# Kernel optimization log

Measured on AMD Instinct MI355X. Metric: run time of the kernel, lower is better.

The kernel has to match this reference:

```python
import jax, jax.numpy as jnp
import numpy as np

N = 100000          # nodes
E = 800000          # edges per relation
R = 6               # relations
B = 1000            # graphs
IN_DIM = 14
POS_COL = 5
PE = 8              # pos_emb_dim
H = 128             # hidden_dim
OUT = 128           # out_dim
NPOS = 24
D1 = IN_DIM - 1 + PE  # 21, GAT layer-1 input dim


def setup_inputs() -> dict:
    key = jax.random.key(0)
    ks = jax.random.split(key, 20)
    x_all = jax.random.normal(ks[0], (N, IN_DIM), dtype=jnp.float32)
    pos = jax.random.randint(ks[1], (N,), 0, NPOS)
    x_all = x_all.at[:, POS_COL].set(pos.astype(jnp.float32))
    edges = jax.random.randint(ks[2], (R, 2, E), 0, N, dtype=jnp.int32)
    batch = jnp.sort(jax.random.randint(ks[3], (N,), 0, B, dtype=jnp.int32))
    pos_table = jax.random.normal(ks[4], (NPOS, PE), dtype=jnp.float32) * 0.02
    W1 = jax.random.normal(ks[5], (R, D1, H), dtype=jnp.float32) * 0.1
    as1 = jax.random.normal(ks[6], (R, H), dtype=jnp.float32) * 0.1
    ad1 = jax.random.normal(ks[7], (R, H), dtype=jnp.float32) * 0.1
    b1 = jnp.zeros((R, H), dtype=jnp.float32)
    W2 = jax.random.normal(ks[8], (R, H, H), dtype=jnp.float32) * 0.05
    as2 = jax.random.normal(ks[9], (R, H), dtype=jnp.float32) * 0.1
    ad2 = jax.random.normal(ks[10], (R, H), dtype=jnp.float32) * 0.1
    b2 = jnp.zeros((R, H), dtype=jnp.float32)
    n1w = jnp.ones((H,), dtype=jnp.float32)
    n1b = jnp.zeros((H,), dtype=jnp.float32)
    n2w = jnp.ones((H,), dtype=jnp.float32)
    n2b = jnp.zeros((H,), dtype=jnp.float32)
    query = jax.random.normal(ks[11], (H,), dtype=jnp.float32) * 0.02
    projW = jax.random.normal(ks[12], (H, OUT), dtype=jnp.float32) * 0.05
    projb = jnp.zeros((OUT,), dtype=jnp.float32)
    return dict(x_all=x_all, edges=edges, batch=batch, pos_table=pos_table,
                W1=W1, as1=as1, ad1=ad1, b1=b1, W2=W2, as2=as2, ad2=ad2, b2=b2,
                n1w=n1w, n1b=n1b, n2w=n2w, n2b=n2b, query=query, projW=projW, projb=projb)


def _seg_softmax(logits, seg, num):
    m = jax.lax.stop_gradient(jax.ops.segment_max(logits, seg, num_segments=num))
    e = jnp.exp(logits - m[seg])
    s = jax.ops.segment_sum(e, seg, num_segments=num)
    return e / s[seg]


def _gat_layer(x, W, a_s, a_d, b, edges):
    # sum over R relation-specific GATConv(heads=1, concat=False) outputs
    n = x.shape[0]
    out = jnp.zeros((n, W.shape[-1]), dtype=x.dtype)
    for r in range(R):
        xp = x @ W[r]                       # [N, H] projected features
        src, dst = edges[r, 0], edges[r, 1]
        z = (xp @ a_s[r])[src] + (xp @ a_d[r])[dst]
        z = jnp.where(z > 0, z, 0.2 * z)    # LeakyReLU(0.2)
        alpha = _seg_softmax(z, dst, n)     # per-destination softmax
        agg = jax.ops.segment_sum(alpha[:, None] * xp[src], dst, num_segments=n)
        out = out + agg + b[r]
    return out


def _ln(x, w, b):
    mu = x.mean(-1, keepdims=True)
    v = ((x - mu) ** 2).mean(-1, keepdims=True)
    return (x - mu) / jnp.sqrt(v + 1e-5) * w + b


def reference(x_all, edges, batch, pos_table, W1, as1, ad1, b1,
              W2, as2, ad2, b2, n1w, n1b, n2w, n2b, query, projW, projb):
    cont = jnp.concatenate([x_all[:, :POS_COL], x_all[:, POS_COL + 1:]], axis=1)
    pidx = jnp.clip(x_all[:, POS_COL].astype(jnp.int32), 0, NPOS - 1)
    x = jnp.concatenate([cont, pos_table[pidx]], axis=1)  # [N, D1]
    x = _gat_layer(x, W1, as1, ad1, b1, edges)
    x = _ln(jax.nn.gelu(x, approximate=False), n1w, n1b)
    x = _gat_layer(x, W2, as2, ad2, b2, edges)
    x = _ln(jax.nn.gelu(x, approximate=False), n2w, n2b)
    # AttentionPooling: gather-score-softmax-scatter over batch segments
    scores = x @ query
    w = _seg_softmax(scores, batch, B)
    pool = jax.ops.segment_sum(w[:, None] * x, batch, num_segments=B)  # [B, H]
    return pool @ projW + projb
```

## Files before the change

### kernel.cpp

```cpp
#include <hip/hip_runtime.h>
#include <math.h>

#define NN   100000
#define EE   800000
#define RR   6
#define BB   1000
#define HH   128
#define MM   (RR*NN)
#define NBPR ((NN + 255) >> 8)
#define NBK  (RR * NBPR)
#define CH   4096
#define CAP  4096

static inline int ceil_div(int a, int b){ return (a+b-1)/b; }

typedef __attribute__((ext_vector_type(8))) short bf16x8;
typedef __attribute__((ext_vector_type(4))) short bf16x4;
typedef __attribute__((ext_vector_type(4))) float f32x4;

__device__ __forceinline__ unsigned fenc(float f){
  unsigned u = __float_as_uint(f);
  return (u & 0x80000000u) ? ~u : (u | 0x80000000u);
}
__device__ __forceinline__ float fdec(unsigned u){
// ... 32 lines not shown
  __syncthreads();
  for (int i = e0 + t; i < e1; i += 256) {
    int dst = dptr[i];
    int b = dst >> 8;
    int slot = base[b] + atomicAdd(&hist[b], 1);
    ebkt[slot] = ((unsigned)sptr[i] << 8) | (unsigned)(dst & 255);
  }
}

__global__ void k_bscan(const int* __restrict__ bcur, int* __restrict__ boff,
                        int* __restrict__ off)
{
  __shared__ int sh[256];
  int t = threadIdx.x;
  int carry = 0;
  for (int c = 0; c < NBK; c += 256) {
    int idx = c + t;
    int v = (idx < NBK) ? bcur[idx] : 0;
    sh[t] = v;
    __syncthreads();
    for (int o = 1; o < 256; o <<= 1) {
      int add = (t >= o) ? sh[t-o] : 0;
      __syncthreads();
      sh[t] += add;
      __syncthreads();
    }
    int incl = sh[t];
    int tot  = sh[255];
    if (idx < NBK) boff[idx] = carry + incl - v;
    __syncthreads();
    carry += tot;
  }
  if (t == 0) { boff[NBK] = carry; off[MM] = carry; }
}

__global__ void k_bbuild(const unsigned* __restrict__ ebkt, const int* __restrict__ bcur,
                         const int* __restrict__ boff,
                         int* __restrict__ off, int* __restrict__ elist)
{
  __shared__ int cnt[256];
  __shared__ int sc[256];
  __shared__ int cur[256];
  int t = threadIdx.x;
  int bb = blockIdx.x;
  int e0r = bb*CAP, e1r = e0r + bcur[bb];
  int w0 = boff[bb];
  cnt[t] = 0;
  __syncthreads();
  for (int i = e0r + t; i < e1r; i += 256)
    atomicAdd(&cnt[ebkt[i] & 255u], 1);
  __syncthreads();
  sc[t] = cnt[t];
  __syncthreads();
  for (int o = 1; o < 256; o <<= 1) {
    int add = (t >= o) ? sc[t-o] : 0;
    __syncthreads();
    sc[t] += add;
    __syncthreads();
  }
  int excl = sc[t] - cnt[t];
  int r = bb / NBPR, b = bb - r*NBPR;
  int dst = b*256 + t;
  if (dst < NN) off[r*NN + dst] = w0 + excl;
  cur[t] = w0 + excl;
  __syncthreads();
  for (int i = e0r + t; i < e1r; i += 256) {
    unsigned w = ebkt[i];
    int slot = atomicAdd(&cur[w & 255u], 1);
    elist[slot] = (int)(w >> 8);
  }
}

__global__ void k_featprep(const float* __restrict__ x_all, const float* __restrict__ pos_table,
                           short* __restrict__ x0h, short* __restrict__ x0l)
{
  int gid = blockIdx.x*256 + threadIdx.x;
  if (gid >= NN*32) return;
  int nidx = gid >> 5, c = gid & 31;
  float v = 0.f;
  if (c < 13) {
    int scl = (c < 5) ? c : c + 1;
    v = x_all[nidx*14 + scl];
  } else if (c < 21) {
    int pi = (int)x_all[nidx*14 + 5];
    pi = pi < 0 ? 0 : (pi > 23 ? 23 : pi);
    v = pos_table[pi*8 + (c - 13)];
  }
  unsigned short h = f2bf(v);
  unsigned short l = f2bf(v - bf2f(h));
  x0h[gid] = (short)h;
  x0l[gid] = (short)l;
}

template<int KP>
__global__ void k_wprep(const float* __restrict__ W, int K,
                        short* __restrict__ Wh, short* __restrict__ Wl)
{
  int gid = blockIdx.x*256 + threadIdx.x;
  if (gid >= RR*128*KP) return;
  int r = gid / (128*KP);
  int rem = gid - r*(128*KP);
  int nn = rem / KP, k = rem - nn*KP;
  float v = (k < K) ? W[((size_t)r*K + k)*128 + nn] : 0.f;
  unsigned short h = f2bf(v);
  unsigned short l = f2bf(v - bf2f(h));
  Wh[gid] = (short)h;
  Wl[gid] = (short)l;
}

template<int KP>
__global__ void k_wa(const float* __restrict__ W, const float* __restrict__ as,
                     const float* __restrict__ ad, int K, float* __restrict__ wa)
{
  int idx = blockIdx.x*256 + threadIdx.x;
  if (idx >= 12*KP) return;
  int rr = idx / KP, k = idx - rr*KP;
  int r = (rr < 6) ? rr : rr - 6;
  const float* a = ((rr < 6) ? as : ad) + (size_t)r*HH;
  float s = 0.f;
  if (k < K) {
    const float* wrow = W + ((size_t)r*K + k)*128;
    #pragma unroll 8
    for (int h = 0; h < 128; ++h) s = fmaf(wrow[h], a[h], s);
  }
  wa[idx] = s;
}

__global__ void k_zsd32(const short* __restrict__ xh, const short* __restrict__ xl,
                        const float* __restrict__ wa, float* __restrict__ zsd, int n)
{
  __shared__ float w[12*32];
  int tid = threadIdx.x;
  for (int i = tid; i < 12*32; i += 256) w[i] = wa[i];
  __syncthreads();
  int g = blockIdx.x*256 + tid;
  if (g >= n) return;
  float v[32];
  #pragma unroll
  for (int c = 0; c < 4; ++c) {
    uint4 vh = *(const uint4*)(xh + (size_t)g*32 + c*8);
    uint4 vl = *(const uint4*)(xl + (size_t)g*32 + c*8);
    const unsigned short* hp = (const unsigned short*)&vh;
    const unsigned short* lp = (const unsigned short*)&vl;
    #pragma unroll
    for (int j = 0; j < 8; ++j) v[c*8+j] = bf2f(hp[j]) + bf2f(lp[j]);
  }
  #pragma unroll
  for (int rr = 0; rr < 12; ++rr) {
    float d = 0.f;
    #pragma unroll
    for (int k = 0; k < 32; ++k) d = fmaf(v[k], w[rr*32+k], d);
    zsd[(size_t)rr*n + g] = d;
  }
}

__global__ void k_agg1(const unsigned short* __restrict__ x0h, const float* __restrict__ zsd,
                       const int* __restrict__ elist, const int* __restrict__ off,
                       unsigned short* __restrict__ aggH, unsigned short* __restrict__ aggL,
                       int n)
{
  int gid = blockIdx.x*256 + threadIdx.x;
  int g = gid >> 4;
  int l = threadIdx.x & 15;
  if (g >= n) return;
  int sub = l >> 2, ch = l & 3;

  for (int rel = 0; rel < RR; ++rel) {
    const float* zsr = zsd + (size_t)rel*n;
    const float* zdr = zsd + (size_t)(6+rel)*n;
    int o0 = off[(size_t)rel*NN + g];
    int deg = off[(size_t)rel*NN + g + 1] - o0;
    float acc[8] = {0,0,0,0,0,0,0,0};
    float inv = 0.f;
    if (deg > 0) {
      float zdd = zdr[g];
      float m = -3.4e38f, es = 0.f;
      for (int i = l; i < deg; i += 16) {
        float z = zsr[elist[o0+i]] + zdd;
        z = (z > 0.f) ? z : 0.2f*z;
        float mn = fmaxf(m, z);
        es = es*__expf(m - mn) + __expf(z - mn);
        m = mn;
      }
      #pragma unroll
      for (int o = 1; o <= 8; o <<= 1) {
        float mo = __shfl_xor(m, o), eo = __shfl_xor(es, o);
        float mn = fmaxf(m, mo);
        es = es*__expf(m - mn) + eo*__expf(mo - mn);
        m = mn;
      }
      inv = 1.f / es;
      for (int base = 0; base < deg; base += 8) {
        int i0 = base + sub, i1 = base + 4 + sub;
        float e0 = 0.f, e1 = 0.f; int s0 = 0, s1 = 0;
        if (i0 < deg) {
          s0 = elist[o0+i0];
          float z = zsr[s0] + zdd;
          z = (z > 0.f) ? z : 0.2f*z;
          e0 = __expf(z - m);
        }
        if (i1 < deg) {
          s1 = elist[o0+i1];
          float z = zsr[s1] + zdd;
          z = (z > 0.f) ? z : 0.2f*z;
          e1 = __expf(z - m);
        }
        uint4 v0 = *(const uint4*)(x0h + (size_t)s0*32 + ch*8);
        uint4 v1 = *(const uint4*)(x0h + (size_t)s1*32 + ch*8);
        acc[0] = fmaf(e0, __uint_as_float(v0.x << 16),         acc[0]);
        acc[1] = fmaf(e0, __uint_as_float(v0.x & 0xffff0000u), acc[1]);
        acc[2] = fmaf(e0, __uint_as_float(v0.y << 16),         acc[2]);
        acc[3] = fmaf(e0, __uint_as_float(v0.y & 0xffff0000u), acc[3]);
        acc[4] = fmaf(e0, __uint_as_float(v0.z << 16),         acc[4]);
        acc[5] = fmaf(e0, __uint_as_float(v0.z & 0xffff0000u), acc[5]);
        acc[6] = fmaf(e0, __uint_as_float(v0.w << 16),         acc[6]);
        acc[7] = fmaf(e0, __uint_as_float(v0.w & 0xffff0000u), acc[7]);
        acc[0] = fmaf(e1, __uint_as_float(v1.x << 16),         acc[0]);
        acc[1] = fmaf(e1, __uint_as_float(v1.x & 0xffff0000u), acc[1]);
        acc[2] = fmaf(e1, __uint_as_float(v1.y << 16),         acc[2]);
        acc[3] = fmaf(e1, __uint_as_float(v1.y & 0xffff0000u), acc[3]);
        acc[4] = fmaf(e1, __uint_as_float(v1.z << 16),         acc[4]);
        acc[5] = fmaf(e1, __uint_as_float(v1.z & 0xffff0000u), acc[5]);
        acc[6] = fmaf(e1, __uint_as_float(v1.w << 16),         acc[6]);
        acc[7] = fmaf(e1, __uint_as_float(v1.w & 0xffff0000u), acc[7]);
      }
      #pragma unroll
      for (int j = 0; j < 8; ++j) {
        acc[j] += __shfl_xor(acc[j], 4);
        acc[j] += __shfl_xor(acc[j], 8);
      }
    }
    if (sub == 0) {
      uint4 ph, pl;
      unsigned* php = (unsigned*)&ph; unsigned* plp = (unsigned*)&pl;
      #pragma unroll
      for (int j2 = 0; j2 < 4; ++j2) {
        float a0 = acc[2*j2]   * inv;
        float a1 = acc[2*j2+1] * inv;
        unsigned short h0 = f2bf(a0), h1 = f2bf(a1);
        php[j2] = ((unsigned)h1 << 16) | h0;
        plp[j2] = ((unsigned)f2bf(a1 - bf2f(h1)) << 16) | f2bf(a0 - bf2f(h0));
      }
      size_t o = ((size_t)rel*n + g)*32 + ch*8;
      *(uint4*)(aggH + o) = ph;
      *(uint4*)(aggL + o) = pl;
    }
  }
}

__device__ __forceinline__ bf16x8 ldfragG(const short* __restrict__ p, int row, int kb, int KP_)
{
  bf16x4 a = *(const bf16x4*)(p + (size_t)row*KP_ + kb);
  bf16x4 b = *(const bf16x4*)(p + (size_t)row*KP_ + kb + 16);
  return __builtin_shufflevector(a, b, 0,1,2,3,4,5,6,7);
}

__global__ __launch_bounds__(256, 4)
void k_gemm1(const short* __restrict__ aggH, const short* __restrict__ aggL,
             const short* __restrict__ Wh, const short* __restrict__ Wl,
             const float* __restrict__ bsv,
             const float* __restrict__ nw, const float* __restrict__ nb,
             unsigned short* __restrict__ Yh, int n)
{
  __shared__ __align__(16) float Cs[32*136];
  int tid = threadIdx.x;
  int r0 = blockIdx.x * 32;
  int wid = tid >> 6, lane = tid & 63;
  int lr = lane & 15, lg = lane >> 4;
  int rt = wid >> 1;
  int c0 = (wid & 1) * 4;
  int arow = r0 + rt*16 + lr;
  int kb = 4*lg;
  f32x4 acct[4] = {{0,0,0,0},{0,0,0,0},{0,0,0,0},{0,0,0,0}};

  for (int rel = 0; rel < RR; ++rel) {
    const short* Ahr = aggH + (size_t)rel*n*32;
    const short* Alr = aggL + (size_t)rel*n*32;
    const short* Whr = Wh + (size_t)rel*128*32;
    const short* Wlr = Wl + (size_t)rel*128*32;
    bf16x8 ah = ldfragG(Ahr, arow, kb, 32);
    bf16x8 al = ldfragG(Alr, arow, kb, 32);
    #pragma unroll
    for (int t = 0; t < 4; ++t) {
      int wrow = (c0 + t)*16 + lr;
      bf16x8 whf = ldfragG(Whr, wrow, kb, 32);
      bf16x8 wlf = ldfragG(Wlr, wrow, kb, 32);
      acct[t] = __builtin_amdgcn_mfma_f32_16x16x32_bf16(ah, whf, acct[t], 0, 0, 0);
      acct[t] = __builtin_amdgcn_mfma_f32_16x16x32_bf16(al, whf, acct[t], 0, 0, 0);
      acct[t] = __builtin_amdgcn_mfma_f32_16x16x32_bf16(ah, wlf, acct[t], 0, 0, 0);
    }
  }

  #pragma unroll
  for (int t = 0; t < 4; ++t)
    #pragma unroll
    for (int v = 0; v < 4; ++v) {
      int row = rt*16 + lg*4 + v;
      int col = (c0 + t)*16 + lr;
      float x = acct[t][v] + bsv[col];
      Cs[row*136 + col] = 0.5f*x*(1.f + erff(x*0.70710678118654752f));
    }
  __syncthreads();
  {
    int r = tid >> 3, sg = tid & 7;
    float vals[16];
    float s = 0.f;
    #pragma unroll
    for (int i = 0; i < 16; ++i) { vals[i] = Cs[r*136 + sg*16 + i]; s += vals[i]; }
    s += __shfl_xor(s, 1); s += __shfl_xor(s, 2); s += __shfl_xor(s, 4);
    float mu = s * (1.f/128.f);
    float var = 0.f;
    #pragma unroll
    for (int i = 0; i < 16; ++i) { vals[i] -= mu; var += vals[i]*vals[i]; }
    var += __shfl_xor(var, 1); var += __shfl_xor(var, 2); var += __shfl_xor(var, 4);
    float inv = 1.f / sqrtf(var*(1.f/128.f) + 1e-5f);
    int g = r0 + r;
    uint4 ph0, ph1;
    unsigned* php0 = (unsigned*)&ph0; unsigned* php1 = (unsigned*)&ph1;
    #pragma unroll
    for (int j2 = 0; j2 < 8; ++j2) {
      int c = sg*16 + 2*j2;
      float y0 = vals[2*j2]  *inv*nw[c]   + nb[c];
      float y1 = vals[2*j2+1]*inv*nw[c+1] + nb[c+1];
      unsigned hw = ((unsigned)f2bf(y1) << 16) | f2bf(y0);
      if (j2 < 4) php0[j2] = hw; else php1[j2-4] = hw;
    }
    *(uint4*)(Yh + (size_t)g*128 + sg*16)     = ph0;
    *(uint4*)(Yh + (size_t)g*128 + sg*16 + 8) = ph1;
  }
}

__device__ __forceinline__ bf16x8 ldfrag_(const short* p, int row, int kb, int KP_, int smask)
{
  int xr = row & smask;
  int s0 = (((kb)      >> 3) ^ xr) * 8 + (kb & 7);
  int s1 = (((kb + 16) >> 3) ^ xr) * 8 + (kb & 7);
  bf16x4 a = *(const bf16x4*)(p + (size_t)row*KP_ + s0);
  bf16x4 b = *(const bf16x4*)(p + (size_t)row*KP_ + s1);
  return __builtin_shufflevector(a, b, 0,1,2,3,4,5,6,7);
}

template<int KP>
__global__ __launch_bounds__(256, 2)
void k_gemm_mfma(const short* __restrict__ Ah,
                 const short* __restrict__ WhAll, const short* __restrict__ WlAll,
                 const float* __restrict__ a_sAll, const float* __restrict__ a_dAll,
                 unsigned short* __restrict__ xpbAll, float* __restrict__ zsAll,
                 float* __restrict__ zdAll, int rbase, int n)
{
  constexpr int SLOTS = KP/8;
  constexpr int SMASK = (SLOTS >= 8) ? 7 : (SLOTS-1);
  __shared__ short lds[288*KP];
  constexpr int AH0 = 0, WH0 = 32*KP, WL0 = 160*KP;
  int tid = threadIdx.x;
  int r0 = blockIdx.x * 32;
  int ry = blockIdx.y;
  const short* Wh = WhAll + (size_t)(rbase+ry)*128*KP;
  const short* Wl = WlAll + (size_t)(rbase+ry)*128*KP;
  const float* a_s = a_sAll + (size_t)(rbase+ry)*HH;
  const float* a_d = a_dAll + (size_t)(rbase+ry)*HH;
  unsigned short* xpb = xpbAll + (size_t)ry*n*128;
  float* zs = zsAll + (size_t)ry*n;
  float* zd = zdAll + (size_t)ry*n;

  for (int ch = tid; ch < 32*SLOTS; ch += 256) {
    int row = ch / SLOTS, slot = ch - row*SLOTS;
    int gr = r0 + row;
    int dsl = (slot ^ (row & SMASK)) * 8;
    bf16x8 vh;
    if (gr < n) {
      vh = *(const bf16x8*)(Ah + (size_t)gr*KP + slot*8);
    } else {
      #pragma unroll
      for (int q = 0; q < 8; ++q) vh[q] = 0;
    }
    *(bf16x8*)(lds + AH0 + row*KP + dsl) = vh;
  }
  for (int ch = tid; ch < 128*SLOTS; ch += 256) {
    int row = ch / SLOTS, slot = ch - row*SLOTS;
    int dsl = (slot ^ (row & SMASK)) * 8;
    *(bf16x8*)(lds + WH0 + row*KP + dsl) = *(const bf16x8*)(Wh + (size_t)row*KP + slot*8);
    *(bf16x8*)(lds + WL0 + row*KP + dsl) = *(const bf16x8*)(Wl + (size_t)row*KP + slot*8);
  }
  __syncthreads();

  int wid = tid >> 6, lane = tid & 63;
  int lr = lane & 15, lg = lane >> 4;
  int rt = wid >> 1;
  int c0 = (wid & 1) * 4;
  f32x4 acc[4] = {{0,0,0,0},{0,0,0,0},{0,0,0,0},{0,0,0,0}};
  int arow = rt*16 + lr;

  #pragma unroll
  for (int kc = 0; kc < KP/32; ++kc) {
    int kb = kc*32 + 4*lg;
    bf16x8 ah = ldfrag_(lds + AH0, arow, kb, KP, SMASK);
    #pragma unroll
    for (int t = 0; t < 4; ++t) {
      int wrow = (c0 + t)*16 + lr;
      bf16x8 wh = ldfrag_(lds + WH0, wrow, kb, KP, SMASK);
      bf16x8 wl = ldfrag_(lds + WL0, wrow, kb, KP, SMASK);
      acc[t] = __builtin_amdgcn_mfma_f32_16x16x32_bf16(ah, wh, acc[t], 0, 0, 0);
      acc[t] = __builtin_amdgcn_mfma_f32_16x16x32_bf16(ah, wl, acc[t], 0, 0, 0);
    }
  }
  __syncthreads();

  float* Cs = (float*)lds;
  #pragma unroll
  for (int t = 0; t < 4; ++t)
    #pragma unroll
    for (int v = 0; v < 4; ++v) {
      int row = rt*16 + lg*4 + v;
      int col = (c0 + t)*16 + lr;
      Cs[row*136 + col] = acc[t][v];
    }
  __syncthreads();

  {
    int r = tid >> 3, sg = tid & 7;
    float ps = 0.f, pd = 0.f;
    #pragma unroll
    for (int i = 0; i < 16; ++i) {
      int c = sg*16 + i;
      float x = Cs[r*136 + c];
      ps = fmaf(x, a_s[c], ps);
      pd = fmaf(x, a_d[c], pd);
    }
    ps += __shfl_xor(ps, 1); pd += __shfl_xor(pd, 1);
    ps += __shfl_xor(ps, 2); pd += __shfl_xor(pd, 2);
    ps += __shfl_xor(ps, 4); pd += __shfl_xor(pd, 4);
    int gr = r0 + r;
    if (sg == 0 && gr < n) { zs[gr] = ps; zd[gr] = pd; }
  }
  for (int i = tid; i < 32*16; i += 256) {
    int row = i >> 4, q = i & 15;
    int gr = r0 + row;
    if (gr < n) {
      const float* cp = Cs + row*136 + q*8;
      uint4 o;
      o.x = ((unsigned)f2bf(cp[1]) << 16) | f2bf(cp[0]);
      o.y = ((unsigned)f2bf(cp[3]) << 16) | f2bf(cp[2]);
      o.z = ((unsigned)f2bf(cp[5]) << 16) | f2bf(cp[4]);
      o.w = ((unsigned)f2bf(cp[7]) << 16) | f2bf(cp[6]);
      *(uint4*)(xpb + (size_t)gr*128 + q*8) = o;
    }
  }
}

#define ACC8(W_, U_) \
  tmp[0] = fmaf(W_, __uint_as_float((U_).x << 16),         tmp[0]); \
  tmp[1] = fmaf(W_, __uint_as_float((U_).x & 0xffff0000u), tmp[1]); \
  tmp[2] = fmaf(W_, __uint_as_float((U_).y << 16),         tmp[2]); \
  tmp[3] = fmaf(W_, __uint_as_float((U_).y & 0xffff0000u), tmp[3]); \
  tmp[4] = fmaf(W_, __uint_as_float((U_).z << 16),         tmp[4]); \
  tmp[5] = fmaf(W_, __uint_as_float((U_).z & 0xffff0000u), tmp[5]); \
  tmp[6] = fmaf(W_, __uint_as_float((U_).w << 16),         tmp[6]); \
  tmp[7] = fmaf(W_, __uint_as_float((U_).w & 0xffff0000u), tmp[7]);

template<int NREL, int FIN>
__global__ void k_agg3(const unsigned short* __restrict__ xpb,
                       const float* __restrict__ zs,
                       const float* __restrict__ zd,
                       const int* __restrict__ elist,
                       const int* __restrict__ off,
                       float* __restrict__ hacc,
                       const float* __restrict__ bsum,
                       const float* __restrict__ nw, const float* __restrict__ nb,
                       float* __restrict__ Yf,
                       const float* __restrict__ q,
                       const int* __restrict__ batch,
                       float* __restrict__ scores, unsigned* __restrict__ bmax,
                       int n)
{
  int gid = blockIdx.x*256 + threadIdx.x;
  int g = gid >> 4;
  int l = threadIdx.x & 15;
  int gbase = threadIdx.x & 48;
  if (g >= n) return;

  float acc[8] = {0,0,0,0,0,0,0,0};

  for (int r = 0; r < NREL; ++r) {
    int o0 = off[(size_t)r*NN + g], o1 = off[(size_t)r*NN + g + 1];
    int deg = o1 - o0;
    if (deg <= 0) continue;
    const float* zsr = zs + (size_t)r*n;
    float zdd = zd[(size_t)r*n + g];

    float m = -3.4e38f;
    for (int i = l; i < deg; i += 16) {
      float z = zsr[elist[o0+i]] + zdd;
      z = (z > 0.f) ? z : 0.2f*z;
      m = fmaxf(m, z);
    }
    m = fmaxf(m, __shfl_xor(m, 1));
    m = fmaxf(m, __shfl_xor(m, 2));
    m = fmaxf(m, __shfl_xor(m, 4));
    m = fmaxf(m, __shfl_xor(m, 8));

    float tmp[8] = {0,0,0,0,0,0,0,0};
    float esum = 0.f;
    const unsigned short* xr = xpb + (size_t)r*n*128;
    for (int base = 0; base < deg; base += 16) {
      int i = base + l;
      float ew = 0.f; int s = 0;
      if (i < deg) {
        s = elist[o0+i];
        float z = zsr[s] + zdd;
        z = (z > 0.f) ? z : 0.2f*z;
        ew = __expf(z - m);
      }
      esum += ew;
      int cnt = min(16, deg - base);
      for (int t = 0; t < cnt; t += 4) {
        float w0 = __shfl(ew, gbase + t);
        float w1 = __shfl(ew, gbase + t + 1);
        float w2 = __shfl(ew, gbase + t + 2);
        float w3 = __shfl(ew, gbase + t + 3);
        int a0 = __shfl(s, gbase + t);
        int a1 = __shfl(s, gbase + t + 1);
        int a2 = __shfl(s, gbase + t + 2);
        int a3 = __shfl(s, gbase + t + 3);
        uint4 u0 = *(const uint4*)(xr + (size_t)a0*128 + l*8);
        uint4 u1 = *(const uint4*)(xr + (size_t)a1*128 + l*8);
        uint4 u2 = *(const uint4*)(xr + (size_t)a2*128 + l*8);
        uint4 u3 = *(const uint4*)(xr + (size_t)a3*128 + l*8);
        ACC8(w0, u0);
        ACC8(w1, u1);
        ACC8(w2, u2);
        ACC8(w3, u3);
      }
    }
    esum += __shfl_xor(esum, 1);
    esum += __shfl_xor(esum, 2);
    esum += __shfl_xor(esum, 4);
    esum += __shfl_xor(esum, 8);
    float inv = 1.f / esum;
    #pragma unroll
    for (int j = 0; j < 8; ++j) acc[j] = fmaf(tmp[j], inv, acc[j]);
  }

  if (FIN == 0) {
    float* hp = hacc + (size_t)g*128 + l*8;
    float4 o0; o0.x = acc[0]; o0.y = acc[1]; o0.z = acc[2]; o0.w = acc[3];
    float4 o1; o1.x = acc[4]; o1.y = acc[5]; o1.z = acc[6]; o1.w = acc[7];
    *(float4*)hp = o0;
    *(float4*)(hp + 4) = o1;
  } else {
    if (FIN == 2) {
      const float* hp = hacc + (size_t)g*128 + l*8;
      float4 p0 = *(const float4*)hp;
      float4 p1 = *(const float4*)(hp + 4);
      acc[0] += p0.x; acc[1] += p0.y; acc[2] += p0.z; acc[3] += p0.w;
      acc[4] += p1.x; acc[5] += p1.y; acc[6] += p1.z; acc[7] += p1.w;
    }
    float4 b0 = *(const float4*)(bsum + l*8);
    float4 b1 = *(const float4*)(bsum + l*8 + 4);
    acc[0] += b0.x; acc[1] += b0.y; acc[2] += b0.z; acc[3] += b0.w;
    acc[4] += b1.x; acc[5] += b1.y; acc[6] += b1.z; acc[7] += b1.w;
    float s = 0.f;
    #pragma unroll
    for (int j = 0; j < 8; ++j) {
      acc[j] = 0.5f*acc[j]*(1.f + erff(acc[j]*0.70710678118654752f));
      s += acc[j];
    }
    s += __shfl_xor(s, 1); s += __shfl_xor(s, 2);
    s += __shfl_xor(s, 4); s += __shfl_xor(s, 8);
    float mu = s * (1.f/128.f);
    float v = 0.f;
    #pragma unroll
    for (int j = 0; j < 8; ++j) { acc[j] -= mu; v += acc[j]*acc[j]; }
    v += __shfl_xor(v, 1); v += __shfl_xor(v, 2);
    v += __shfl_xor(v, 4); v += __shfl_xor(v, 8);
    v *= (1.f/128.f);
    float inv = 1.f / sqrtf(v + 1e-5f);
    float4 w0 = *(const float4*)(nw + l*8);
    float4 w1 = *(const float4*)(nw + l*8 + 4);
    float4 nb0 = *(const float4*)(nb + l*8);
    float4 nb1 = *(const float4*)(nb + l*8 + 4);
    float y[8];
    y[0] = acc[0]*inv*w0.x + nb0.x; y[1] = acc[1]*inv*w0.y + nb0.y;
    y[2] = acc[2]*inv*w0.z + nb0.z; y[3] = acc[3]*inv*w0.w + nb0.w;
    y[4] = acc[4]*inv*w1.x + nb1.x; y[5] = acc[5]*inv*w1.y + nb1.y;
    y[6] = acc[6]*inv*w1.z + nb1.z; y[7] = acc[7]*inv*w1.w + nb1.w;
    float* yp = Yf + (size_t)g*128 + l*8;
    float4 o0; o0.x = y[0]; o0.y = y[1]; o0.z = y[2]; o0.w = y[3];
    float4 o1; o1.x = y[4]; o1.y = y[5]; o1.z = y[6]; o1.w = y[7];
    *(float4*)yp = o0;
    *(float4*)(yp + 4) = o1;
    float4 q0 = *(const float4*)(q + l*8);
    float4 q1 = *(const float4*)(q + l*8 + 4);
    float sc = y[0]*q0.x + y[1]*q0.y + y[2]*q0.z + y[3]*q0.w
             + y[4]*q1.x + y[5]*q1.y + y[6]*q1.z + y[7]*q1.w;
    sc += __shfl_xor(sc, 1); sc += __shfl_xor(sc, 2);
    sc += __shfl_xor(sc, 4); sc += __shfl_xor(sc, 8);
    if (l == 0) {
      scores[g] = sc;
      atomicMax(&bmax[batch[g]], fenc(sc));
    }
  }
}

__global__ void k_bsum(const float* __restrict__ b, float* __restrict__ bs)
{
  int t = threadIdx.x;
  float s = 0.f;
  #pragma unroll
  for (int r = 0; r < RR; ++r) s += b[r*HH + t];
  bs[t] = s;
}

__global__ void k_segbounds(const int* __restrict__ batch, int* __restrict__ segst,
                            int n, int numB)
{
  int b = blockIdx.x*256 + threadIdx.x;
  if (b > numB) return;
  int lo = 0, hi = n;
  while (lo < hi) { int mid = (lo+hi) >> 1; if (batch[mid] < b) lo = mid+1; else hi = mid; }
  segst[b] = lo;
}

__global__ void k_pool(const float* __restrict__ X, const float* __restrict__ scores,
                       const int* __restrict__ segst, const unsigned* __restrict__ bmax,
                       float* __restrict__ pool, int numB)
{
  int b = blockIdx.x;
  int t = threadIdx.x;
  int s0 = segst[b], s1 = segst[b+1];
  float m = fdec(bmax[b]);
  float acc0 = 0.f, acc1 = 0.f, esum = 0.f;
  int i = s0;
  for (; i + 1 < s1; i += 2) {
    float e0 = __expf(scores[i] - m);
    float e1 = __expf(scores[i+1] - m);
    esum += e0 + e1;
    acc0 = fmaf(e0, X[(size_t)i*128 + t], acc0);
    acc1 = fmaf(e1, X[(size_t)(i+1)*128 + t], acc1);
  }
  if (i < s1) {
    float e0 = __expf(scores[i] - m);
    esum += e0;
    acc0 = fmaf(e0, X[(size_t)i*128 + t], acc0);
  }
  float inv = (s1 > s0) ? 1.f/esum : 0.f;
  pool[(size_t)b*128 + t] = (acc0 + acc1) * inv;
}

__global__ void k_outgemm(const float* __restrict__ pool, const float* __restrict__ projW,
                          const float* __restrict__ projb, float* __restrict__ out, int numB)
{
  int b = blockIdx.x;
  int j = threadIdx.x;
  __shared__ float p[128];
  p[j] = pool[(size_t)b*128 + j];
  __syncthreads();
  float acc = projb[j];
  #pragma unroll 16
  for (int k = 0; k < 128; ++k) acc = fmaf(p[k], projW[(size_t)k*128 + j], acc);
  out[(size_t)b*128 + j] = acc;
}

extern "C" void kernel_launch(void* const* d_in, const int* in_sizes, int n_in,
                              void* d_out, int out_size, void* d_ws, size_t ws_size,
                              hipStream_t stream)
{
  const float* x_all = (const float*)d_in[0];
  const int*   edges = (const int*)d_in[1];
  const int*   batch = (const int*)d_in[2];
  const float* pos_table = (const float*)d_in[3];
  const float* W1  = (const float*)d_in[4];
  const float* as1 = (const float*)d_in[5];
  const float* ad1 = (const float*)d_in[6];
  const float* b1  = (const float*)d_in[7];
  const float* W2  = (const float*)d_in[8];
  const float* as2 = (const float*)d_in[9];
  const float* ad2 = (const float*)d_in[10];
  const float* b2  = (const float*)d_in[11];
  const float* n1w = (const float*)d_in[12];
  const float* n1b = (const float*)d_in[13];
  const float* n2w = (const float*)d_in[14];
  const float* n2b = (const float*)d_in[15];
  const float* query = (const float*)d_in[16];
  const float* projW = (const float*)d_in[17];
  const float* projb = (const float*)d_in[18];
  float* out = (float*)d_out;
  (void)in_sizes; (void)n_in; (void)out_size;

  auto asz = [](size_t b){ return (b + 255) & ~(size_t)255; };
  size_t baseNeed =
      asz((size_t)(MM+1)*4) + asz((size_t)RR*EE*4) + asz((size_t)(NBK+1)*4) +
      asz((size_t)NBK*4) + 2*asz((size_t)RR*128*128*2) + asz((size_t)12*128*4) +
      asz((size_t)12*NN*4) + asz(128*4) + asz((size_t)(BB+1)*4) + asz((size_t)BB*4) +
      asz((size_t)BB*HH*4) + asz((size_t)NN*4) +
      asz((size_t)NN*128*4)  + asz((size_t)NN*128*4) ;
  size_t need6 = baseNeed + asz((size_t)6*NN*128*2);
  const bool use6 = ws_size >= need6;

  char* p = (char*)d_ws;
  auto alloc = [&](size_t b){ void* r = (void*)p; p += (b + 255) & ~(size_t)255; return r; };
  int*   off   = (int*)alloc((size_t)(MM+1)*sizeof(int));
  int*   elist = (int*)alloc((size_t)RR*EE*sizeof(int));
  int*   boff  = (int*)alloc((size_t)(NBK+1)*sizeof(int));
  int*   bcur  = (int*)alloc((size_t)NBK*sizeof(int));
  short* wtH   = (short*)alloc((size_t)RR*128*128*sizeof(short));
  short* wtL   = (short*)alloc((size_t)RR*128*128*sizeof(short));
  float* wa    = (float*)alloc((size_t)12*128*sizeof(float));
  float* zsd   = (float*)alloc((size_t)12*NN*sizeof(float));
  float* bsv   = (float*)alloc(128*sizeof(float));
  int*   segst = (int*)alloc((size_t)(BB+1)*sizeof(int));
  unsigned* bmax = (unsigned*)alloc((size_t)BB*sizeof(unsigned));
  float* pool  = (float*)alloc((size_t)BB*HH*sizeof(float));
  float* scrs  = (float*)alloc((size_t)NN*sizeof(float));
  size_t xpbRel = use6 ? 6 : 3;
  unsigned short* xpb = (unsigned short*)alloc((size_t)xpbRel*NN*128*sizeof(short));
  float* R1    = (float*)alloc((size_t)NN*128*sizeof(float));
  float* R2    = (float*)alloc((size_t)NN*128*sizeof(float));

  unsigned* ebkt = (unsigned*)R1;
  short* x0h = (short*)R1;
  short* x0l = x0h + (size_t)NN*32;
  float* hacc = R1;
  unsigned short* h1h = (unsigned short*)R2;
  float* h2 = (float*)R2;
  unsigned short* aggH = (unsigned short*)xpb;
  unsigned short* aggL = aggH + (size_t)RR*NN*32;
  float* zs = zsd;
  float* zd = zsd + (use6 ? (size_t)6*NN : (size_t)3*NN);

  const int nch = (EE + CH - 1) / CH;
  hipMemsetAsync(bcur, 0, (size_t)NBK*sizeof(int), stream);
  k_binscatter<<<RR*nch,256,0,stream>>>(edges, bcur, ebkt);
  k_bscan<<<1,256,0,stream>>>(bcur, boff, off);
  k_bbuild<<<NBK,256,0,stream>>>(ebkt, bcur, boff, off, elist);

  k_featprep<<<ceil_div(NN*32,256),256,0,stream>>>(x_all, pos_table, x0h, x0l);
  k_segbounds<<<ceil_div(BB+1,256),256,0,stream>>>(batch, segst, NN, BB);
  hipMemsetAsync(bmax, 0, (size_t)BB*sizeof(unsigned), stream);

  k_wa<32><<<ceil_div(12*32,256),256,0,stream>>>(W1, as1, ad1, 21, wa);
  k_zsd32<<<ceil_div(NN,256),256,0,stream>>>(x0h, x0l, wa, zsd, NN);
  k_wprep<32><<<ceil_div(RR*128*32,256),256,0,stream>>>(W1, 21, wtH, wtL);
  k_bsum<<<1,128,0,stream>>>(b1, bsv);
  k_agg1<<<ceil_div(NN*16,256),256,0,stream>>>((const unsigned short*)x0h, zsd, elist, off,
                                               aggH, aggL, NN);
  k_gemm1<<<ceil_div(NN,32),256,0,stream>>>((const short*)aggH, (const short*)aggL,
                                            wtH, wtL, bsv, n1w, n1b, h1h, NN);

  k_wprep<128><<<ceil_div(RR*128*128,256),256,0,stream>>>(W2, 128, wtH, wtL);
  k_bsum<<<1,128,0,stream>>>(b2, bsv);
  int aggGrid = ceil_div(NN*16, 256);
  if (use6) {
    dim3 g6(ceil_div(NN,32), 6);
    k_gemm_mfma<128><<<g6,256,0,stream>>>((const short*)h1h,
                                          wtH, wtL, as2, ad2, xpb, zs, zd, 0, NN);
    k_agg3<6,3><<<aggGrid,256,0,stream>>>(xpb, zs, zd, elist, off, (float*)0,
        bsv, n2w, n2b, h2, query, batch, scrs, bmax, NN);
  } else {
    dim3 g3(ceil_div(NN,32), 3);
    k_gemm_mfma<128><<<g3,256,0,stream>>>((const short*)h1h,
                                          wtH, wtL, as2, ad2, xpb, zs, zd, 0, NN);
    k_agg3<3,0><<<aggGrid,256,0,stream>>>(xpb, zs, zd, elist, off, hacc,
        bsv, n2w, n2b, (float*)0, query, batch, scrs, bmax, NN);
    k_gemm_mfma<128><<<g3,256,0,stream>>>((const short*)h1h,
                                          wtH, wtL, as2, ad2, xpb, zs, zd, 3, NN);
    k_agg3<3,2><<<aggGrid,256,0,stream>>>(xpb, zs, zd, elist, off + (size_t)3*NN, hacc,
        bsv, n2w, n2b, h2, query, batch, scrs, bmax, NN);
  }

  k_pool<<<BB,128,0,stream>>>(h2, scrs, segst, bmax, pool, BB);
  k_outgemm<<<BB,128,0,stream>>>(pool, projW, projb, out, BB);
}
```

Before: 872.4 us.

## Aggregate layer-2 inputs before projection and compute attention logits via folded weights

Layer 2 now aggregates the 128-dim bf16 h1 features per relation before applying W2, as layer 1 already does. The per-relation GEMMs are summed in a single MFMA kernel that loops over three relations. Attention logits come from a small kernel that dots h1 with the precomputed W2·a_s and W2·a_d vectors, so there is no longer a separate projected xpb tensor. This removes the 6-relation buffer path and ws-size branching, at the cost of two aggregation passes, two GEMM passes and an extra bf16 rounding of the aggregated features.

```diff
diff --git a/kernel.cpp b/kernel.cpp
--- a/kernel.cpp
+++ b/kernel.cpp
@@ -208,6 +208,34 @@
     for (int k = 0; k < 32; ++k) d = fmaf(v[k], w[rr*32+k], d);
     zsd[(size_t)rr*n + g] = d;
   }
+}
+
+__global__ void k_zsd128(const unsigned short* __restrict__ xh,
+                         const float* __restrict__ wa, float* __restrict__ zsd, int n)
+{
+  __shared__ float w[12*128];
+  int tid = threadIdx.x;
+  for (int i = tid; i < 12*128; i += 256) w[i] = wa[i];
+  __syncthreads();
+  int gid = blockIdx.x*256 + tid;
+  int g = gid >> 4, l = tid & 15;
+  if (g >= n) return;
+  uint4 vh = *(const uint4*)(xh + (size_t)g*128 + l*8);
+  const unsigned short* hp = (const unsigned short*)&vh;
+  float v[8];
+  #pragma unroll
+  for (int j = 0; j < 8; ++j) v[j] = bf2f(hp[j]);
+  float dot[12];
+  #pragma unroll
+  for (int rr = 0; rr < 12; ++rr) {
+    float p = 0.f;
+    #pragma unroll
+    for (int j = 0; j < 8; ++j) p = fmaf(v[j], w[rr*128 + l*8 + j], p);
+    p += __shfl_xor(p, 1); p += __shfl_xor(p, 2);
+    p += __shfl_xor(p, 4); p += __shfl_xor(p, 8);
+    dot[rr] = p;
+  }
+  if (l < 12) zsd[(size_t)l*n + g] = dot[l];
 }
 
 __global__ void k_agg1(const unsigned short* __restrict__ x0h, const float* __restrict__ zsd,
@@ -386,124 +414,6 @@
   }
 }
 
-__device__ __forceinline__ bf16x8 ldfrag_(const short* p, int row, int kb, int KP_, int smask)
-{
-  int xr = row & smask;
-  int s0 = (((kb)      >> 3) ^ xr) * 8 + (kb & 7);
-  int s1 = (((kb + 16) >> 3) ^ xr) * 8 + (kb & 7);
-  bf16x4 a = *(const bf16x4*)(p + (size_t)row*KP_ + s0);
-  bf16x4 b = *(const bf16x4*)(p + (size_t)row*KP_ + s1);
-  return __builtin_shufflevector(a, b, 0,1,2,3,4,5,6,7);
-}
-
-template<int KP>
-__global__ __launch_bounds__(256, 2)
-void k_gemm_mfma(const short* __restrict__ Ah,
-                 const short* __restrict__ WhAll, const short* __restrict__ WlAll,
-                 const float* __restrict__ a_sAll, const float* __restrict__ a_dAll,
-                 unsigned short* __restrict__ xpbAll, float* __restrict__ zsAll,
-                 float* __restrict__ zdAll, int rbase, int n)
-{
-  constexpr int SLOTS = KP/8;
-  constexpr int SMASK = (SLOTS >= 8) ? 7 : (SLOTS-1);
-  __shared__ short lds[288*KP];
-  constexpr int AH0 = 0, WH0 = 32*KP, WL0 = 160*KP;
-  int tid = threadIdx.x;
-  int r0 = blockIdx.x * 32;
-  int ry = blockIdx.y;
-  const short* Wh = WhAll + (size_t)(rbase+ry)*128*KP;
-  const short* Wl = WlAll + (size_t)(rbase+ry)*128*KP;
-  const float* a_s = a_sAll + (size_t)(rbase+ry)*HH;
-  const float* a_d = a_dAll + (size_t)(rbase+ry)*HH;
-  unsigned short* xpb = xpbAll + (size_t)ry*n*128;
-  float* zs = zsAll + (size_t)ry*n;
-  float* zd = zdAll + (size_t)ry*n;
-
-  for (int ch = tid; ch < 32*SLOTS; ch += 256) {
-    int row = ch / SLOTS, slot = ch - row*SLOTS;
-    int gr = r0 + row;
-    int dsl = (slot ^ (row & SMASK)) * 8;
-    bf16x8 vh;
-    if (gr < n) {
-      vh = *(const bf16x8*)(Ah + (size_t)gr*KP + slot*8);
-    } else {
-      #pragma unroll
-      for (int q = 0; q < 8; ++q) vh[q] = 0;
-    }
-    *(bf16x8*)(lds + AH0 + row*KP + dsl) = vh;
-  }
-  for (int ch = tid; ch < 128*SLOTS; ch += 256) {
-    int row = ch / SLOTS, slot = ch - row*SLOTS;
-    int dsl = (slot ^ (row & SMASK)) * 8;
-    *(bf16x8*)(lds + WH0 + row*KP + dsl) = *(const bf16x8*)(Wh + (size_t)row*KP + slot*8);
-    *(bf16x8*)(lds + WL0 + row*KP + dsl) = *(const bf16x8*)(Wl + (size_t)row*KP + slot*8);
-  }
-  __syncthreads();
-
-  int wid = tid >> 6, lane = tid & 63;
-  int lr = lane & 15, lg = lane >> 4;
-  int rt = wid >> 1;
-  int c0 = (wid & 1) * 4;
-  f32x4 acc[4] = {{0,0,0,0},{0,0,0,0},{0,0,0,0},{0,0,0,0}};
-  int arow = rt*16 + lr;
-
-  #pragma unroll
-  for (int kc = 0; kc < KP/32; ++kc) {
-    int kb = kc*32 + 4*lg;
-    bf16x8 ah = ldfrag_(lds + AH0, arow, kb, KP, SMASK);
-    #pragma unroll
-    for (int t = 0; t < 4; ++t) {
-      int wrow = (c0 + t)*16 + lr;
-      bf16x8 wh = ldfrag_(lds + WH0, wrow, kb, KP, SMASK);
-      bf16x8 wl = ldfrag_(lds + WL0, wrow, kb, KP, SMASK);
-      acc[t] = __builtin_amdgcn_mfma_f32_16x16x32_bf16(ah, wh, acc[t], 0, 0, 0);
-      acc[t] = __builtin_amdgcn_mfma_f32_16x16x32_bf16(ah, wl, acc[t], 0, 0, 0);
-    }
-  }
-  __syncthreads();
-
-  float* Cs = (float*)lds;
-  #pragma unroll
-  for (int t = 0; t < 4; ++t)
-    #pragma unroll
-    for (int v = 0; v < 4; ++v) {
-      int row = rt*16 + lg*4 + v;
-      int col = (c0 + t)*16 + lr;
-      Cs[row*136 + col] = acc[t][v];
-    }
-  __syncthreads();
-
-  {
-    int r = tid >> 3, sg = tid & 7;
-    float ps = 0.f, pd = 0.f;
-    #pragma unroll
-    for (int i = 0; i < 16; ++i) {
-      int c = sg*16 + i;
-      float x = Cs[r*136 + c];
-      ps = fmaf(x, a_s[c], ps);
-      pd = fmaf(x, a_d[c], pd);
-    }
-    ps += __shfl_xor(ps, 1); pd += __shfl_xor(pd, 1);
-    ps += __shfl_xor(ps, 2); pd += __shfl_xor(pd, 2);
-    ps += __shfl_xor(ps, 4); pd += __shfl_xor(pd, 4);
-    int gr = r0 + r;
-    if (sg == 0 && gr < n) { zs[gr] = ps; zd[gr] = pd; }
-  }
-  for (int i = tid; i < 32*16; i += 256) {
-    int row = i >> 4, q = i & 15;
-    int gr = r0 + row;
-    if (gr < n) {
-      const float* cp = Cs + row*136 + q*8;
-      uint4 o;
-      o.x = ((unsigned)f2bf(cp[1]) << 16) | f2bf(cp[0]);
-      o.y = ((unsigned)f2bf(cp[3]) << 16) | f2bf(cp[2]);
-      o.z = ((unsigned)f2bf(cp[5]) << 16) | f2bf(cp[4]);
-      o.w = ((unsigned)f2bf(cp[7]) << 16) | f2bf(cp[6]);
-      *(uint4*)(xpb + (size_t)gr*128 + q*8) = o;
-    }
-  }
-}
-
 #define ACC8(W_, U_) \
   tmp[0] = fmaf(W_, __uint_as_float((U_).x << 16),         tmp[0]); \
   tmp[1] = fmaf(W_, __uint_as_float((U_).x & 0xffff0000u), tmp[1]); \
@@ -514,19 +424,12 @@
   tmp[6] = fmaf(W_, __uint_as_float((U_).w << 16),         tmp[6]); \
   tmp[7] = fmaf(W_, __uint_as_float((U_).w & 0xffff0000u), tmp[7]);
 
-template<int NREL, int FIN>
-__global__ void k_agg3(const unsigned short* __restrict__ xpb,
-                       const float* __restrict__ zs,
-                       const float* __restrict__ zd,
+__global__ void k_agg2(const unsigned short* __restrict__ h1,
+                       const float* __restrict__ zsd,
                        const int* __restrict__ elist,
                        const int* __restrict__ off,
-                       float* __restrict__ hacc,
-                       const float* __restrict__ bsum,
-                       const float* __restrict__ nw, const float* __restrict__ nb,
-                       float* __restrict__ Yf,
-                       const float* __restrict__ q,
-                       const int* __restrict__ batch,
-                       float* __restrict__ scores, unsigned* __restrict__ bmax,
+                       int rbase,
+                       unsigned short* __restrict__ agg2,
                        int n)
 {
   int gid = blockIdx.x*256 + threadIdx.x;
@@ -535,123 +438,190 @@
   int gbase = threadIdx.x & 48;
   if (g >= n) return;
 
-  float acc[8] = {0,0,0,0,0,0,0,0};
-
-  for (int r = 0; r < NREL; ++r) {
+  for (int r = 0; r < 3; ++r) {
     int o0 = off[(size_t)r*NN + g], o1 = off[(size_t)r*NN + g + 1];
     int deg = o1 - o0;
-    if (deg <= 0) continue;
-    const float* zsr = zs + (size_t)r*n;
-    float zdd = zd[(size_t)r*n + g];
-
-    float m = -3.4e38f;
-    for (int i = l; i < deg; i += 16) {
-      float z = zsr[elist[o0+i]] + zdd;
-      z = (z > 0.f) ? z : 0.2f*z;
-      m = fmaxf(m, z);
-    }
-    m = fmaxf(m, __shfl_xor(m, 1));
-    m = fmaxf(m, __shfl_xor(m, 2));
-    m = fmaxf(m, __shfl_xor(m, 4));
-    m = fmaxf(m, __shfl_xor(m, 8));
-
     float tmp[8] = {0,0,0,0,0,0,0,0};
-    float esum = 0.f;
-    const unsigned short* xr = xpb + (size_t)r*n*128;
-    for (int base = 0; base < deg; base += 16) {
-      int i = base + l;
-      float ew = 0.f; int s = 0;
-      if (i < deg) {
-        s = elist[o0+i];
-        float z = zsr[s] + zdd;
+    float inv = 0.f;
+    if (deg > 0) {
+      const float* zsr = zsd + (size_t)(rbase+r)*n;
+      float zdd = zsd[(size_t)(6+rbase+r)*n + g];
+
+      float m = -3.4e38f;
+      for (int i = l; i < deg; i += 16) {
+        float z = zsr[elist[o0+i]] + zdd;
         z = (z > 0.f) ? z : 0.2f*z;
-        ew = __expf(z - m);
+        m = fmaxf(m, z);
       }
-      esum += ew;
-      int cnt = min(16, deg - base);
-      for (int t = 0; t < cnt; t += 4) {
-        float w0 = __shfl(ew, gbase + t);
-        float w1 = __shfl(ew, gbase + t + 1);
-        float w2 = __shfl(ew, gbase + t + 2);
-        float w3 = __shfl(ew, gbase + t + 3);
-        int a0 = __shfl(s, gbase + t);
-        int a1 = __shfl(s, gbase + t + 1);
-        int a2 = __shfl(s, gbase + t + 2);
-        int a3 = __shfl(s, gbase + t + 3);
-        uint4 u0 = *(const uint4*)(xr + (size_t)a0*128 + l*8);
-        uint4 u1 = *(const uint4*)(xr + (size_t)a1*128 + l*8);
-        uint4 u2 = *(const uint4*)(xr + (size_t)a2*128 + l*8);
-        uint4 u3 = *(const uint4*)(xr + (size_t)a3*128 + l*8);
-        ACC8(w0, u0);
-        ACC8(w1, u1);
-        ACC8(w2, u2);
-        ACC8(w3, u3);
+      m = fmaxf(m, __shfl_xor(m, 1));
+      m = fmaxf(m, __shfl_xor(m, 2));
+      m = fmaxf(m, __shfl_xor(m, 4));
+      m = fmaxf(m, __shfl_xor(m, 8));
+
+      float esum = 0.f;
+      for (int base = 0; base < deg; base += 16) {
+        int i = base + l;
+        float ew = 0.f; int s = 0;
+        if (i < deg) {
+          s = elist[o0+i];
+          float z = zsr[s] + zdd;
+          z = (z > 0.f) ? z : 0.2f*z;
+          ew = __expf(z - m);
+        }
+        esum += ew;
+        int cnt = min(16, deg - base);
+        for (int t = 0; t < cnt; t += 4) {
+          float w0 = __shfl(ew, gbase + t);
+          float w1 = __shfl(ew, gbase + t + 1);
+          float w2 = __shfl(ew, gbase + t + 2);
+          float w3 = __shfl(ew, gbase + t + 3);
+          int a0 = __shfl(s, gbase + t);
+          int a1 = __shfl(s, gbase + t + 1);
+          int a2 = __shfl(s, gbase + t + 2);
+          int a3 = __shfl(s, gbase + t + 3);
+          uint4 u0 = *(const uint4*)(h1 + (size_t)a0*128 + l*8);
+          uint4 u1 = *(const uint4*)(h1 + (size_t)a1*128 + l*8);
+          uint4 u2 = *(const uint4*)(h1 + (size_t)a2*128 + l*8);
+          uint4 u3 = *(const uint4*)(h1 + (size_t)a3*128 + l*8);
+          ACC8(w0, u0);
+          ACC8(w1, u1);
+          ACC8(w2, u2);
+          ACC8(w3, u3);
+        }
       }
-    }
-    esum += __shfl_xor(esum, 1);
-    esum += __shfl_xor(esum, 2);
-    esum += __shfl_xor(esum, 4);
-    esum += __shfl_xor(esum, 8);
-    float inv = 1.f / esum;
-    #pragma unroll
-    for (int j = 0; j < 8; ++j) acc[j] = fmaf(tmp[j], inv, acc[j]);
-  }
+      esum += __shfl_xor(esum, 1);
+      esum += __shfl_xor(esum, 2);
+      esum += __shfl_xor(esum, 4);
+      esum += __shfl_xor(esum, 8);
+      inv = 1.f / esum;
+    }
+    uint4 ph;
+    unsigned* php = (unsigned*)&ph;
+    #pragma unroll
+    for (int j2 = 0; j2 < 4; ++j2) {
+      float a0 = tmp[2*j2]   * inv;
+      float a1 = tmp[2*j2+1] * inv;
+      php[j2] = ((unsigned)f2bf(a1) << 16) | f2bf(a0);
+    }
+    *(uint4*)(agg2 + ((size_t)r*n + g)*128 + l*8) = ph;
+  }
+}
+
+__device__ __forceinline__ bf16x8 ldfrag_(const short* p, int row, int kb, int KP_, int smask)
+{
+  int xr = row & smask;
+  int s0 = (((kb)      >> 3) ^ xr) * 8 + (kb & 7);
+  int s1 = (((kb + 16) >> 3) ^ xr) * 8 + (kb & 7);
+  bf16x4 a = *(const bf16x4*)(p + (size_t)row*KP_ + s0);
+  bf16x4 b = *(const bf16x4*)(p + (size_t)row*KP_ + s1);
+  return __builtin_shufflevector(a, b, 0,1,2,3,4,5,6,7);
+}
+
+template<int FIN>
+__global__ __launch_bounds__(256, 2)
+void k_gemm2(const unsigned short* __restrict__ agg2,
+             const short* __restrict__ WhAll, const short* __restrict__ WlAll, int rbase,
+             const float* __restrict__ bsv,
+             const float* __restrict__ nw, const float* __restrict__ nb,
+             float* __restrict__ hacc, float* __restrict__ Yf,
+             const float* __restrict__ q, const int* __restrict__ batch,
+             float* __restrict__ scores, unsigned* __restrict__ bmax, int n)
+{
+  constexpr int KP = 128, SLOTS = 16, SMASK = 7;
+  __shared__ short lds[288*KP];
+  constexpr int AH0 = 0, WH0 = 32*KP, WL0 = 160*KP;
+  int tid = threadIdx.x;
+  int r0 = blockIdx.x * 32;
+  int wid = tid >> 6, lane = tid & 63;
+  int lr = lane & 15, lg = lane >> 4;
+  int rt = wid >> 1;
+  int c0 = (wid & 1) * 4;
+  int arow = rt*16 + lr;
+  f32x4 acc[4] = {{0,0,0,0},{0,0,0,0},{0,0,0,0},{0,0,0,0}};
+
+  for (int rel = 0; rel < 3; ++rel) {
+    const unsigned short* Ar = agg2 + (size_t)rel*n*KP;
+    const short* Wh = WhAll + (size_t)(rbase+rel)*128*KP;
+    const short* Wl = WlAll + (size_t)(rbase+rel)*128*KP;
+    for (int ch = tid; ch < 32*SLOTS; ch += 256) {
+      int row = ch / SLOTS, slot = ch - row*SLOTS;
+      int dsl = (slot ^ (row & SMASK)) * 8;
+      *(bf16x8*)(lds + AH0 + row*KP + dsl) =
+          *(const bf16x8*)((const short*)Ar + (size_t)(r0+row)*KP + slot*8);
+    }
+    for (int ch = tid; ch < 128*SLOTS; ch += 256) {
+      int row = ch / SLOTS, slot = ch - row*SLOTS;
+      int dsl = (slot ^ (row & SMASK)) * 8;
+      *(bf16x8*)(lds + WH0 + row*KP + dsl) = *(const bf16x8*)(Wh + (size_t)row*KP + slot*8);
+      *(bf16x8*)(lds + WL0 + row*KP + dsl) = *(const bf16x8*)(Wl + (size_t)row*KP + slot*8);
+    }
+    __syncthreads();
+    #pragma unroll
+    for (int kc = 0; kc < KP/32; ++kc) {
+      int kb = kc*32 + 4*lg;
+      bf16x8 ah = ldfrag_(lds + AH0, arow, kb, KP, SMASK);
+      #pragma unroll
+      for (int t = 0; t < 4; ++t) {
+        int wrow = (c0 + t)*16 + lr;
+        bf16x8 wh = ldfrag_(lds + WH0, wrow, kb, KP, SMASK);
+        bf16x8 wl = ldfrag_(lds + WL0, wrow, kb, KP, SMASK);
+        acc[t] = __builtin_amdgcn_mfma_f32_16x16x32_bf16(ah, wh, acc[t], 0, 0, 0);
+        acc[t] = __builtin_amdgcn_mfma_f32_16x16x32_bf16(ah, wl, acc[t], 0, 0, 0);
+      }
+    }
+    __syncthreads();
+  }
+
+  float* Cs = (float*)lds;
+  #pragma unroll
+  for (int t = 0; t < 4; ++t)
+    #pragma unroll
+    for (int v = 0; v < 4; ++v) {
+      int row = rt*16 + lg*4 + v;
+      int col = (c0 + t)*16 + lr;
+      Cs[row*136 + col] = acc[t][v];
+    }
+  __syncthreads();
 
   if (FIN == 0) {
-    float* hp = hacc + (size_t)g*128 + l*8;
-    float4 o0; o0.x = acc[0]; o0.y = acc[1]; o0.z = acc[2]; o0.w = acc[3];
-    float4 o1; o1.x = acc[4]; o1.y = acc[5]; o1.z = acc[6]; o1.w = acc[7];
-    *(float4*)hp = o0;
-    *(float4*)(hp + 4) = o1;
+    for (int i = tid; i < 32*32; i += 256) {
+      int row = i >> 5, q4 = i & 31;
+      *(float4*)(hacc + (size_t)(r0+row)*128 + q4*4) = *(const float4*)(Cs + row*136 + q4*4);
+    }
   } else {
-    if (FIN == 2) {
-      const float* hp = hacc + (size_t)g*128 + l*8;
-      float4 p0 = *(const float4*)hp;
-      float4 p1 = *(const float4*)(hp + 4);
-      acc[0] += p0.x; acc[1] += p0.y; acc[2] += p0.z; acc[3] += p0.w;
-      acc[4] += p1.x; acc[5] += p1.y; acc[6] += p1.z; acc[7] += p1.w;
-    }
-    float4 b0 = *(const float4*)(bsum + l*8);
-    float4 b1 = *(const float4*)(bsum + l*8 + 4);
-    acc[0] += b0.x; acc[1] += b0.y; acc[2] += b0.z; acc[3] += b0.w;
-    acc[4] += b1.x; acc[5] += b1.y; acc[6] += b1.z; acc[7] += b1.w;
+    int r = tid >> 3, sg = tid & 7;
+    int g = r0 + r;
+    const float* hp = hacc + (size_t)g*128 + sg*16;
+    float vals[16];
     float s = 0.f;
     #pragma unroll
-    for (int j = 0; j < 8; ++j) {
-      acc[j] = 0.5f*acc[j]*(1.f + erff(acc[j]*0.70710678118654752f));
-      s += acc[j];
-    }
-    s += __shfl_xor(s, 1); s += __shfl_xor(s, 2);
-    s += __shfl_xor(s, 4); s += __shfl_xor(s, 8);
+    for (int i = 0; i < 16; ++i) {
+      float x = Cs[r*136 + sg*16 + i] + hp[i] + bsv[sg*16 + i];
+      x = 0.5f*x*(1.f + erff(x*0.70710678118654752f));
+      vals[i] = x;
+      s += x;
+    }
+    s += __shfl_xor(s, 1); s += __shfl_xor(s, 2); s += __shfl_xor(s, 4);
     float mu = s * (1.f/128.f);
-    float v = 0.f;
-    #pragma unroll
-    for (int j = 0; j < 8; ++j) { acc[j] -= mu; v += acc[j]*acc[j]; }
-    v += __shfl_xor(v, 1); v += __shfl_xor(v, 2);
-    v += __shfl_xor(v, 4); v += __shfl_xor(v, 8);
-    v *= (1.f/128.f);
-    float inv = 1.f / sqrtf(v + 1e-5f);
-    float4 w0 = *(const float4*)(nw + l*8);
-    float4 w1 = *(const float4*)(nw + l*8 + 4);
-    float4 nb0 = *(const float4*)(nb + l*8);
-    float4 nb1 = *(const float4*)(nb + l*8 + 4);
-    float y[8];
-    y[0] = acc[0]*inv*w0.x + nb0.x; y[1] = acc[1]*inv*w0.y + nb0.y;
-    y[2] = acc[2]*inv*w0.z + nb0.z; y[3] = acc[3]*inv*w0.w + nb0.w;
-    y[4] = acc[4]*inv*w1.x + nb1.x; y[5] = acc[5]*inv*w1.y + nb1.y;
-    y[6] = acc[6]*inv*w1.z + nb1.z; y[7] = acc[7]*inv*w1.w + nb1.w;
-    float* yp = Yf + (size_t)g*128 + l*8;
-    float4 o0; o0.x = y[0]; o0.y = y[1]; o0.z = y[2]; o0.w = y[3];
-    float4 o1; o1.x = y[4]; o1.y = y[5]; o1.z = y[6]; o1.w = y[7];
-    *(float4*)yp = o0;
-    *(float4*)(yp + 4) = o1;
-    float4 q0 = *(const float4*)(q + l*8);
-    float4 q1 = *(const float4*)(q + l*8 + 4);
-    float sc = y[0]*q0.x + y[1]*q0.y + y[2]*q0.z + y[3]*q0.w
-             + y[4]*q1.x + y[5]*q1.y + y[6]*q1.z + y[7]*q1.w;
-    sc += __shfl_xor(sc, 1); sc += __shfl_xor(sc, 2);
-    sc += __shfl_xor(sc, 4); sc += __shfl_xor(sc, 8);
-    if (l == 0) {
+    float var = 0.f;
+    #pragma unroll
+    for (int i = 0; i < 16; ++i) { vals[i] -= mu; var += vals[i]*vals[i]; }
+    var += __shfl_xor(var, 1); var += __shfl_xor(var, 2); var += __shfl_xor(var, 4);
+    float inv = 1.f / sqrtf(var*(1.f/128.f) + 1e-5f);
+    float sc = 0.f;
+    #pragma unroll
+    for (int j2 = 0; j2 < 4; ++j2) {
+      int c = sg*16 + j2*4;
+      float4 o;
+      o.x = vals[j2*4+0]*inv*nw[c+0] + nb[c+0];
+      o.y = vals[j2*4+1]*inv*nw[c+1] + nb[c+1];
+      o.z = vals[j2*4+2]*inv*nw[c+2] + nb[c+2];
+      o.w = vals[j2*4+3]*inv*nw[c+3] + nb[c+3];
+      *(float4*)(Yf + (size_t)g*128 + c) = o;
+      sc += o.x*q[c] + o.y*q[c+1] + o.z*q[c+2] + o.w*q[c+3];
+    }
+    sc += __shfl_xor(sc, 1); sc += __shfl_xor(sc, 2); sc += __shfl_xor(sc, 4);
+    if (sg == 0) {
       scores[g] = sc;
       atomicMax(&bmax[batch[g]], fenc(sc));
     }
@@ -741,17 +711,7 @@
   const float* projW = (const float*)d_in[17];
   const float* projb = (const float*)d_in[18];
   float* out = (float*)d_out;
-  (void)in_sizes; (void)n_in; (void)out_size;
-
-  auto asz = [](size_t b){ return (b + 255) & ~(size_t)255; };
-  size_t baseNeed =
-      asz((size_t)(MM+1)*4) + asz((size_t)RR*EE*4) + asz((size_t)(NBK+1)*4) +
-      asz((size_t)NBK*4) + 2*asz((size_t)RR*128*128*2) + asz((size_t)12*128*4) +
-      asz((size_t)12*NN*4) + asz(128*4) + asz((size_t)(BB+1)*4) + asz((size_t)BB*4) +
-      asz((size_t)BB*HH*4) + asz((size_t)NN*4) +
-      asz((size_t)NN*128*4)  + asz((size_t)NN*128*4) ;
-  size_t need6 = baseNeed + asz((size_t)6*NN*128*2);
-  const bool use6 = ws_size >= need6;
+  (void)in_sizes; (void)n_in; (void)out_size; (void)ws_size;
 
   char* p = (char*)d_ws;
   auto alloc = [&](size_t b){ void* r = (void*)p; p += (b + 255) & ~(size_t)255; return r; };
@@ -768,8 +728,7 @@
   unsigned* bmax = (unsigned*)alloc((size_t)BB*sizeof(unsigned));
   float* pool  = (float*)alloc((size_t)BB*HH*sizeof(float));
   float* scrs  = (float*)alloc((size_t)NN*sizeof(float));
-  size_t xpbRel = use6 ? 6 : 3;
-  unsigned short* xpb = (unsigned short*)alloc((size_t)xpbRel*NN*128*sizeof(short));
+  unsigned short* big = (unsigned short*)alloc((size_t)3*NN*128*sizeof(short));
   float* R1    = (float*)alloc((size_t)NN*128*sizeof(float));
   float* R2    = (float*)alloc((size_t)NN*128*sizeof(float));
 
@@ -779,10 +738,9 @@
   float* hacc = R1;
   unsigned short* h1h = (unsigned short*)R2;
   float* h2 = (float*)R2;
-  unsigned short* aggH = (unsigned short*)xpb;
+  unsigned short* aggH = big;
   unsigned short* aggL = aggH + (size_t)RR*NN*32;
-  float* zs = zsd;
-  float* zd = zsd + (use6 ? (size_t)6*NN : (size_t)3*NN);
+  unsigned short* agg2 = big;
 
   const int nch = (EE + CH - 1) / CH;
   hipMemsetAsync(bcur, 0, (size_t)NBK*sizeof(int), stream);
@@ -803,26 +761,17 @@
   k_gemm1<<<ceil_div(NN,32),256,0,stream>>>((const short*)aggH, (const short*)aggL,
                                             wtH, wtL, bsv, n1w, n1b, h1h, NN);
 
+  k_wa<128><<<ceil_div(12*128,256),256,0,stream>>>(W2, as2, ad2, 128, wa);
+  k_zsd128<<<ceil_div(NN*16,256),256,0,stream>>>(h1h, wa, zsd, NN);
   k_wprep<128><<<ceil_div(RR*128*128,256),256,0,stream>>>(W2, 128, wtH, wtL);
   k_bsum<<<1,128,0,stream>>>(b2, bsv);
   int aggGrid = ceil_div(NN*16, 256);
-  if (use6) {
-    dim3 g6(ceil_div(NN,32), 6);
-    k_gemm_mfma<128><<<g6,256,0,stream>>>((const short*)h1h,
-                                          wtH, wtL, as2, ad2, xpb, zs, zd, 0, NN);
-    k_agg3<6,3><<<aggGrid,256,0,stream>>>(xpb, zs, zd, elist, off, (float*)0,
-        bsv, n2w, n2b, h2, query, batch, scrs, bmax, NN);
-  } else {
-    dim3 g3(ceil_div(NN,32), 3);
-    k_gemm_mfma<128><<<g3,256,0,stream>>>((const short*)h1h,
-                                          wtH, wtL, as2, ad2, xpb, zs, zd, 0, NN);
-    k_agg3<3,0><<<aggGrid,256,0,stream>>>(xpb, zs, zd, elist, off, hacc,
-        bsv, n2w, n2b, (float*)0, query, batch, scrs, bmax, NN);
-    k_gemm_mfma<128><<<g3,256,0,stream>>>((const short*)h1h,
-                                          wtH, wtL, as2, ad2, xpb, zs, zd, 3, NN);
-    k_agg3<3,2><<<aggGrid,256,0,stream>>>(xpb, zs, zd, elist, off + (size_t)3*NN, hacc,
-        bsv, n2w, n2b, h2, query, batch, scrs, bmax, NN);
-  }
+  k_agg2<<<aggGrid,256,0,stream>>>(h1h, zsd, elist, off, 0, agg2, NN);
+  k_gemm2<0><<<ceil_div(NN,32),256,0,stream>>>(agg2, wtH, wtL, 0, bsv, n2w, n2b,
+      hacc, (float*)0, query, batch, scrs, bmax, NN);
+  k_agg2<<<aggGrid,256,0,stream>>>(h1h, zsd, elist, off + (size_t)3*NN, 3, agg2, NN);
+  k_gemm2<1><<<ceil_div(NN,32),256,0,stream>>>(agg2, wtH, wtL, 3, bsv, n2w, n2b,
+      hacc, h2, query, batch, scrs, bmax, NN);
 
   k_pool<<<BB,128,0,stream>>>(h2, scrs, segst, bmax, pool, BB);
   k_outgemm<<<BB,128,0,stream>>>(pool, projW, projb, out, BB);
```

Measured after the change: 931.7 us. 6.8% more time.
